# Optimization experiments

Measured on AMD Instinct MI355X. Metric: run time of the kernel, lower is better.

Reference implementation:

```python
import jax, jax.numpy as jnp
import numpy as np

P = 16
BN_EPS = 1e-5


def _to_patches(x, c, d):
    # [b, c*P, d*P] -> [b, c*d, P, P]
    b = x.shape[0]
    x = x.reshape(b, c, P, d, P).transpose(0, 1, 3, 2, 4)
    return x.reshape(b, c * d, P, P)


def _dwconv_block(x, dwk, g, bb, m, v, pwk):
    # depthwise 3x3 stride-2 conv (groups=C, no bias) + BN(eval) + GELU + 1x1 pointwise
    C = x.shape[1]
    y = jax.lax.conv_general_dilated(
        x, dwk[:, None, :, :], window_strides=(2, 2), padding=((1, 1), (1, 1)),
        feature_group_count=C, dimension_numbers=('NCHW', 'OIHW', 'NCHW'))
    y = g[None, :, None, None] * (y - m[None, :, None, None]) / jnp.sqrt(v + BN_EPS)[None, :, None, None] + bb[None, :, None, None]
    y = jax.nn.gelu(y, approximate=False)  # torch nn.GELU default = erf
    return jnp.einsum('bchw,oc->bohw', y, pwk)


def _forward(query, key, value, dw_k, bn_g, bn_b, bn_m, bn_v, pw_k, position, c1_w, c1_b, lin_w, lin_b):
    b, units, d_model = query.shape
    c = units // P
    d = d_model // P
    hp = P // 2  # spatial after stride-2 conv
    dk = hp * hp  # d_k = 64

    q = _to_patches(query, c, d)
    k = _to_patches(key, c, d)
    v = _to_patches(value, c, d)

    q = _dwconv_block(q, dw_k[0], bn_g[0], bn_b[0], bn_m[0], bn_v[0], pw_k[0])
    k = _dwconv_block(k, dw_k[1], bn_g[1], bn_b[1], bn_m[1], bn_v[1], pw_k[1])
    v = _dwconv_block(v, dw_k[2], bn_g[2], bn_b[2], bn_m[2], bn_v[2], pw_k[2])

    # [b, c*d, hp, hp] -> [b, c, d, hp*hp]
    q = q.reshape(b, c, d, dk)
    k = k.reshape(b, c, d, dk)
    v = v.reshape(b, c, d, dk)

    scores = jnp.einsum('bcdk,bcek->bcde', q, k) / jnp.sqrt(jnp.asarray(dk, q.dtype))
    scores = scores + position[None]  # learned additive position bias [c,d,d]
    p_attn = jax.nn.softmax(scores, axis=-1)
    x = jnp.einsum('bcde,bcek->bcdk', p_attn, v)  # [b, c, d, dk]

    # 'b c d (p1 p2) -> b (c p1) (d p2)', p1 = P//2
    x = x.reshape(b, c, d, hp, hp).transpose(0, 1, 3, 2, 4).reshape(b, c * hp, d * hp)

    # Conv1d(units//2 -> units, kernel 1) then Linear(d_model//2 -> d_model)
    x = jnp.einsum('bcl,oc->bol', x, c1_w) + c1_b[None, :, None]
    x = jnp.einsum('bcl,ol->bco', x, lin_w) + lin_b[None, None, :]
    return x


def setup_inputs() -> dict:
    key = jax.random.key(0)
    ks = jax.random.split(key, 8)
    b, units, d_model = 64, 32, 4096
    C = (units // P) * (d_model // P)  # 512
    inp = {
        'query': jax.random.normal(ks[0], (b, units, d_model), jnp.float32),
        'key': jax.random.normal(ks[1], (b, units, d_model), jnp.float32),
        'value': jax.random.normal(ks[2], (b, units, d_model), jnp.float32),
        'dw_k': jax.random.normal(ks[3], (3, C, 3, 3), jnp.float32) * 0.1,
        'bn_g': jnp.ones((3, C), jnp.float32),
        'bn_b': jnp.zeros((3, C), jnp.float32),
        'bn_m': jnp.zeros((3, C), jnp.float32),
        'bn_v': jnp.ones((3, C), jnp.float32),
        'pw_k': jax.random.normal(ks[4], (3, C, C), jnp.float32) * 0.02,
        'position': jax.random.normal(ks[5], (units // P, d_model // P, d_model // P), jnp.float32),
        'c1_w': jax.random.normal(ks[6], (units, units // 2), jnp.float32) * 0.1,
        'c1_b': jnp.zeros((units,), jnp.float32),
        'lin_w': jax.random.normal(ks[7], (d_model, d_model // 2), jnp.float32) * 0.02,
        'lin_b': jnp.zeros((d_model,), jnp.float32),
    }
    return inp


def reference(query, key, value, dw_k, bn_g, bn_b, bn_m, bn_v, pw_k, position, c1_w, c1_b, lin_w, lin_b):
    return _forward(query, key, value, dw_k, bn_g, bn_b, bn_m, bn_v, pw_k, position, c1_w, c1_b, lin_w, lin_b)
```

## Files before the change

kernel.cpp:

```cpp
#include <hip/hip_runtime.h>


typedef short s16x8 __attribute__((ext_vector_type(8)));
typedef float f32x4 __attribute__((ext_vector_type(4)));
typedef const __attribute__((address_space(1))) void* gas_t;
typedef __attribute__((address_space(3))) void* las_t;

__device__ __forceinline__ unsigned short f2bf(float x) {
  unsigned u = __float_as_uint(x);
  unsigned r = u + 0x7fffu + ((u >> 16) & 1u);
  return (unsigned short)(r >> 16);
}
__device__ __forceinline__ float bf2f(unsigned short h) {
  return __uint_as_float((unsigned)h << 16);
}

__global__ __launch_bounds__(256) void stageA_kernel(
    const float* __restrict__ xq, const float* __restrict__ xk,
    const float* __restrict__ xv, const float* __restrict__ dwk,
    const float* __restrict__ bng, const float* __restrict__ bnb,
    const float* __restrict__ bnm, const float* __restrict__ bnv,
    unsigned short* __restrict__ tTp)
{
  const int i  = blockIdx.y;
  const float* x = (i == 0) ? xq : (i == 1) ? xk : xv;
  const float* dwk_i = dwk + (size_t)i * 4608;
  const int co = i * 512;
  unsigned short* out = tTp + (size_t)i * 4194304;

  const int dd = threadIdx.x;
  const int oh = blockIdx.x & 7;
  const int cc = (blockIdx.x >> 3) & 1;
  const int b  = blockIdx.x >> 4;
  const int ch = cc * 256 + dd;

  float r[3][16];
#pragma unroll
  for (int kh = 0; kh < 3; ++kh) {
    int ih = 2 * oh - 1 + kh;
    if (ih >= 0 && ih <= 15) {
      const float* p = x + (size_t)(b * 32 + cc * 16 + ih) * 4096 + dd * 16;
#pragma unroll
      for (int jq = 0; jq < 4; ++jq)
        *(float4*)&r[kh][jq * 4] = *(const float4*)(p + jq * 4);
    } else {
#pragma unroll
      for (int j = 0; j < 16; ++j) r[kh][j] = 0.f;
    }
  }
  float w9[9];
#pragma unroll
  for (int j = 0; j < 9; ++j) w9[j] = dwk_i[ch * 9 + j];
  const float scale = bng[co + ch] / sqrtf(bnv[co + ch] + 1e-5f);
  const float shift = bnb[co + ch] - bnm[co + ch] * scale;

#pragma unroll
  for (int ow = 0; ow < 8; ++ow) {
    float acc = 0.f;
#pragma unroll
    for (int kh = 0; kh < 3; ++kh)
#pragma unroll
      for (int kw = 0; kw < 3; ++kw) {
        int iw = 2 * ow - 1 + kw;
        if (iw >= 0 && iw <= 15) acc = fmaf(r[kh][iw], w9[kh * 3 + kw], acc);
      }
    float y = acc * scale + shift;
    y = 0.5f * y * (1.f + erff(y * 0.70710678118654752f));
    unsigned short hi = f2bf(y);
    unsigned short lo = f2bf(y - bf2f(hi));
    size_t rowb = (size_t)(b * 64 + oh * 8 + ow) * 1024;
    out[rowb + ch] = hi;
    out[rowb + 512 + ch] = lo;
  }
}

__global__ __launch_bounds__(256) void split_kernel(
    const float* __restrict__ src, unsigned short* __restrict__ dst,
    int kshift, int total4)
{
  int i = blockIdx.x * 256 + threadIdx.x;
  if (i >= total4) return;
  size_t i4 = (size_t)i * 4;
  int K = 1 << kshift;
  int r = (int)(i4 >> kshift);
  int c = (int)(i4 & (size_t)(K - 1));
  float4 xv = *(const float4*)(src + i4);
  unsigned short h0 = f2bf(xv.x), h1 = f2bf(xv.y), h2 = f2bf(xv.z), h3 = f2bf(xv.w);
  unsigned short l0 = f2bf(xv.x - bf2f(h0)), l1 = f2bf(xv.y - bf2f(h1));
  unsigned short l2 = f2bf(xv.z - bf2f(h2)), l3 = f2bf(xv.w - bf2f(h3));
  unsigned short* dr = dst + (size_t)r * (K * 2) + c;
  uint2 hp, lp;
  hp.x = (unsigned)h0 | ((unsigned)h1 << 16);
  hp.y = (unsigned)h2 | ((unsigned)h3 << 16);
  lp.x = (unsigned)l0 | ((unsigned)l1 << 16);
  lp.y = (unsigned)l2 | ((unsigned)l3 << 16);
  *(uint2*)dr = hp;
  *(uint2*)(dr + K) = lp;
}

__global__ __launch_bounds__(256) void split_rs_kernel(
    const float* __restrict__ src, unsigned short* __restrict__ dst,
    float* __restrict__ rs, int total4)
{
  int i = blockIdx.x * 256 + threadIdx.x;
  if (i >= total4) return;
  size_t i4 = (size_t)i * 4;
  int r = (int)(i4 >> 11);
  int c = (int)(i4 & 2047);
  float4 xv = *(const float4*)(src + i4);
  unsigned short h0 = f2bf(xv.x), h1 = f2bf(xv.y), h2 = f2bf(xv.z), h3 = f2bf(xv.w);
  unsigned short l0 = f2bf(xv.x - bf2f(h0)), l1 = f2bf(xv.y - bf2f(h1));
  unsigned short l2 = f2bf(xv.z - bf2f(h2)), l3 = f2bf(xv.w - bf2f(h3));
  unsigned short* dr = dst + (size_t)r * 4096 + c;
  uint2 hp, lp;
  hp.x = (unsigned)h0 | ((unsigned)h1 << 16);
  hp.y = (unsigned)h2 | ((unsigned)h3 << 16);
  lp.x = (unsigned)l0 | ((unsigned)l1 << 16);
  lp.y = (unsigned)l2 | ((unsigned)l3 << 16);
  *(uint2*)dr = hp;
  *(uint2*)(dr + 2048) = lp;
  float s = xv.x + xv.y + xv.z + xv.w;
#pragma unroll
  for (int off = 1; off < 64; off <<= 1) s += __shfl_xor(s, off, 64);
  if ((threadIdx.x & 63) == 0) atomicAdd(&rs[r], s);
}

__global__ __launch_bounds__(256, 2) void gemm_pw_pipe_kernel(
    const unsigned short* __restrict__ Aall, const unsigned short* __restrict__ Ball,
    unsigned short* __restrict__ Call)
{
  __shared__ unsigned short lds[36864];
  const int t = threadIdx.x;

  const int flat = (blockIdx.z * 8 + blockIdx.y) * 32 + blockIdx.x;
  const int xcd = flat & 7;
  const int ii = flat >> 3;
  const int n0 = (xcd * 4 + (ii & 3)) * 128;
  const int rem = ii >> 2;
  const int m0 = (rem & 7) * 64;
  const int z = rem >> 3;

  const unsigned short* A = Aall + (size_t)z * 524288;
  const unsigned short* B = Ball + (size_t)z * 4194304;
  unsigned short* Cq = Call + (size_t)z * 4194304;

  const int K = 512, twoK = 1024, Km = 511, nt = 24;

  const int lane = t & 63;
  const int wv = t >> 6;
  const int colbase = wv * 32;
  const int h = lane & 15, g = lane >> 4;

  f32x4 acc[4][2];
#pragma unroll
  for (int mf = 0; mf < 4; ++mf)
#pragma unroll
    for (int nf = 0; nf < 2; ++nf)
      acc[mf][nf] = (f32x4){0.f, 0.f, 0.f, 0.f};

  int arow[2], ablk[2], brow[4], bblk[4];
#pragma unroll
  for (int it = 0; it < 2; ++it) {
    int s = it * 256 + t;
    arow[it] = s >> 3;
    ablk[it] = (s & 7) ^ (arow[it] & 7);
  }
#pragma unroll
  for (int it = 0; it < 4; ++it) {
    int s = it * 256 + t;
    brow[it] = s >> 3;
    bblk[it] = (s & 7) ^ (brow[it] & 7);
  }

  auto issueA = [&](int buf, int tt, int it) {
    int kp = tt * 64 + ablk[it] * 8;
    int ac = (kp < twoK) ? (kp & Km) : (kp - K);
    __builtin_amdgcn_global_load_lds(
        (gas_t)(const void*)(A + (size_t)(m0 + arow[it]) * twoK + ac),
        (las_t)(void*)((char*)lds + (buf * 24576 + it * 4096 + t * 16)), 16, 0, 0);
  };
  auto issueB = [&](int buf, int tt, int it) {
    int kp = tt * 64 + bblk[it] * 8;
    int bc = (kp < twoK) ? kp : (kp - twoK);
    __builtin_amdgcn_global_load_lds(
        (gas_t)(const void*)(B + (size_t)(n0 + brow[it]) * twoK + bc),
        (las_t)(void*)((char*)lds + (buf * 24576 + 8192 + it * 4096 + t * 16)), 16, 0, 0);
  };

  int colx[2];
  colx[0] = ((g) ^ (h & 7)) << 4;
  colx[1] = ((4 + g) ^ (h & 7)) << 4;

  auto rdA = [&](int buf, int kk, int mf) -> s16x8 {
    return *(const s16x8*)((const char*)lds +
        (buf * 24576 + (mf * 16 + h) * 128 + colx[kk]));
  };
  auto rdB = [&](int buf, int kk, int nf) -> s16x8 {
    return *(const s16x8*)((const char*)lds +
        (buf * 24576 + 8192 + (colbase + nf * 16 + h) * 128 + colx[kk]));
  };

#define MFMA8(A0, A1, A2, A3, B0, B1) \
  acc[0][0] = __builtin_amdgcn_mfma_f32_16x16x32_bf16(A0, B0, acc[0][0], 0, 0, 0); \
  acc[1][0] = __builtin_amdgcn_mfma_f32_16x16x32_bf16(A1, B0, acc[1][0], 0, 0, 0); \
  acc[2][0] = __builtin_amdgcn_mfma_f32_16x16x32_bf16(A2, B0, acc[2][0], 0, 0, 0); \
  acc[3][0] = __builtin_amdgcn_mfma_f32_16x16x32_bf16(A3, B0, acc[3][0], 0, 0, 0); \
  acc[0][1] = __builtin_amdgcn_mfma_f32_16x16x32_bf16(A0, B1, acc[0][1], 0, 0, 0); \
  acc[1][1] = __builtin_amdgcn_mfma_f32_16x16x32_bf16(A1, B1, acc[1][1], 0, 0, 0); \
  acc[2][1] = __builtin_amdgcn_mfma_f32_16x16x32_bf16(A2, B1, acc[2][1], 0, 0, 0); \
  acc[3][1] = __builtin_amdgcn_mfma_f32_16x16x32_bf16(A3, B1, acc[3][1], 0, 0, 0);

#pragma unroll
  for (int it = 0; it < 2; ++it) issueA(0, 0, it);
#pragma unroll
  for (int it = 0; it < 4; ++it) issueB(0, 0, it);
#pragma unroll
  for (int it = 0; it < 2; ++it) issueA(1, 1, it);
#pragma unroll
  for (int it = 0; it < 4; ++it) issueB(1, 1, it);
  asm volatile("s_waitcnt vmcnt(6)" ::: "memory");
  __builtin_amdgcn_sched_barrier(0);
  __builtin_amdgcn_s_barrier();
  __builtin_amdgcn_sched_barrier(0);

  int bR = 0;
  for (int tt = 0; tt <= nt - 3; ++tt) {
    const int bn2 = (bR >= 1) ? bR - 1 : 2;
    s16x8 a0 = rdA(bR, 0, 0), a1 = rdA(bR, 0, 1), a2 = rdA(bR, 0, 2), a3 = rdA(bR, 0, 3);
    s16x8 b0 = rdB(bR, 0, 0), b1 = rdB(bR, 0, 1);
    issueA(bn2, tt + 2, 0); issueA(bn2, tt + 2, 1); issueB(bn2, tt + 2, 0);
    __builtin_amdgcn_s_barrier();
    __builtin_amdgcn_s_setprio(1);
    MFMA8(a0, a1, a2, a3, b0, b1)
    __builtin_amdgcn_s_setprio(0);
    __builtin_amdgcn_s_barrier();
    a0 = rdA(bR, 1, 0); a1 = rdA(bR, 1, 1); a2 = rdA(bR, 1, 2); a3 = rdA(bR, 1, 3);
    b0 = rdB(bR, 1, 0); b1 = rdB(bR, 1, 1);
    issueB(bn2, tt + 2, 1); issueB(bn2, tt + 2, 2); issueB(bn2, tt + 2, 3);
    __builtin_amdgcn_s_barrier();
    __builtin_amdgcn_s_setprio(1);
    MFMA8(a0, a1, a2, a3, b0, b1)
    __builtin_amdgcn_s_setprio(0);
    asm volatile("s_waitcnt vmcnt(6)" ::: "memory");
    __builtin_amdgcn_sched_barrier(0);
    __builtin_amdgcn_s_barrier();
    __builtin_amdgcn_sched_barrier(0);
    bR = (bR == 2) ? 0 : bR + 1;
  }

  auto compute_tile = [&](int buf) {
#pragma unroll
    for (int kk = 0; kk < 2; ++kk) {
      s16x8 ta0 = rdA(buf, kk, 0), ta1 = rdA(buf, kk, 1);
      s16x8 ta2 = rdA(buf, kk, 2), ta3 = rdA(buf, kk, 3);
      s16x8 tb0 = rdB(buf, kk, 0), tb1 = rdB(buf, kk, 1);
      MFMA8(ta0, ta1, ta2, ta3, tb0, tb1)
    }
  };
  compute_tile(bR);
  __syncthreads();
  compute_tile((bR == 2) ? 0 : bR + 1);
#undef MFMA8

  if (z < 2) {
#pragma unroll
    for (int mf = 0; mf < 4; ++mf) {
      int mbase = m0 + mf * 16 + g * 4;
#pragma unroll
      for (int nf = 0; nf < 2; ++nf) {
        int n = n0 + colbase + nf * 16 + h;
        int bb = n >> 6, d = n & 63;
#pragma unroll
        for (int qq = 0; qq < 4; ++qq) {
          int m = mbase + qq;
          int cc = m >> 8;
          size_t rowb = ((size_t)(bb * 2 + cc) * 256 + (m & 255)) * 128;
          float vvv = acc[mf][nf][qq];
          unsigned short hi = f2bf(vvv);
          unsigned short lo = f2bf(vvv - bf2f(hi));
          Cq[rowb + d] = hi;
          Cq[rowb + 64 + d] = lo;
        }
      }
    }
  } else {
#pragma unroll
    for (int mf = 0; mf < 4; ++mf) {
      int mbase = m0 + mf * 16 + g * 4;
      int cc = mbase >> 8;
      int mc = mbase & 255;
#pragma unroll
      for (int nf = 0; nf < 2; ++nf) {
        int n = n0 + colbase + nf * 16 + h;
        int bb = n >> 6, d = n & 63;
        size_t rowb = ((size_t)(bb * 2 + cc) * 64 + d) * 512;
        ushort4 hv, lv;
        float v0 = acc[mf][nf][0], v1 = acc[mf][nf][1];
        float v2 = acc[mf][nf][2], v3 = acc[mf][nf][3];
        hv.x = f2bf(v0); hv.y = f2bf(v1); hv.z = f2bf(v2); hv.w = f2bf(v3);
        lv.x = f2bf(v0 - bf2f(hv.x)); lv.y = f2bf(v1 - bf2f(hv.y));
        lv.z = f2bf(v2 - bf2f(hv.z)); lv.w = f2bf(v3 - bf2f(hv.w));
        *(ushort4*)&Cq[rowb + mc] = hv;
        *(ushort4*)&Cq[rowb + 256 + mc] = lv;
      }
    }
  }
}

__global__ __launch_bounds__(256, 2) void gemm_final_kernel(
    const unsigned short* __restrict__ A, const unsigned short* __restrict__ B,
    float* __restrict__ C, int M, int N, int K)
{
  __shared__ unsigned short lds[36864];
  const int t = threadIdx.x;

  const int flat = blockIdx.y * 32 + blockIdx.x;
  const int xcd = flat & 7;
  const int ii = flat >> 3;
  const int n0 = (xcd * 4 + (ii & 3)) * 128;
  const int m0 = (ii >> 2) * 64;

  const int twoK = 2 * K, Km = K - 1;
  const int nt = (3 * K) >> 6;

  const int lane = t & 63;
  const int wv = t >> 6;
  const int colbase = wv * 32;
  const int h = lane & 15, g = lane >> 4;

  f32x4 acc[4][2];
#pragma unroll
  for (int mf = 0; mf < 4; ++mf)
#pragma unroll
    for (int nf = 0; nf < 2; ++nf)
      acc[mf][nf] = (f32x4){0.f, 0.f, 0.f, 0.f};

  int arow[2], ablk[2], brow[4], bblk[4];
#pragma unroll
  for (int it = 0; it < 2; ++it) {
    int s = it * 256 + t;
    arow[it] = s >> 3;
    ablk[it] = (s & 7) ^ (arow[it] & 7);
  }
#pragma unroll
  for (int it = 0; it < 4; ++it) {
    int s = it * 256 + t;
    brow[it] = s >> 3;
    bblk[it] = (s & 7) ^ (brow[it] & 7);
  }

  auto issueA = [&](int buf, int tt, int it) {
    int kp = tt * 64 + ablk[it] * 8;
    int ac = (kp < twoK) ? (kp & Km) : (kp - K);
    __builtin_amdgcn_global_load_lds(
        (gas_t)(const void*)(A + (size_t)(m0 + arow[it]) * twoK + ac),
        (las_t)(void*)((char*)lds + (buf * 24576 + it * 4096 + t * 16)), 16, 0, 0);
  };
  auto issueB = [&](int buf, int tt, int it) {
    int kp = tt * 64 + bblk[it] * 8;
    int bc = (kp < twoK) ? kp : (kp - twoK);
    __builtin_amdgcn_global_load_lds(
        (gas_t)(const void*)(B + (size_t)(n0 + brow[it]) * twoK + bc),
        (las_t)(void*)((char*)lds + (buf * 24576 + 8192 + it * 4096 + t * 16)), 16, 0, 0);
  };

  int colx[2];
  colx[0] = ((g) ^ (h & 7)) << 4;
  colx[1] = ((4 + g) ^ (h & 7)) << 4;

  auto rdA = [&](int buf, int kk, int mf) -> s16x8 {
    return *(const s16x8*)((const char*)lds +
        (buf * 24576 + (mf * 16 + h) * 128 + colx[kk]));
  };
  auto rdB = [&](int buf, int kk, int nf) -> s16x8 {
    return *(const s16x8*)((const char*)lds +
        (buf * 24576 + 8192 + (colbase + nf * 16 + h) * 128 + colx[kk]));
  };

#define MFMA8(A0, A1, A2, A3, B0, B1) \
  acc[0][0] = __builtin_amdgcn_mfma_f32_16x16x32_bf16(A0, B0, acc[0][0], 0, 0, 0); \
  acc[1][0] = __builtin_amdgcn_mfma_f32_16x16x32_bf16(A1, B0, acc[1][0], 0, 0, 0); \
  acc[2][0] = __builtin_amdgcn_mfma_f32_16x16x32_bf16(A2, B0, acc[2][0], 0, 0, 0); \
  acc[3][0] = __builtin_amdgcn_mfma_f32_16x16x32_bf16(A3, B0, acc[3][0], 0, 0, 0); \
  acc[0][1] = __builtin_amdgcn_mfma_f32_16x16x32_bf16(A0, B1, acc[0][1], 0, 0, 0); \
  acc[1][1] = __builtin_amdgcn_mfma_f32_16x16x32_bf16(A1, B1, acc[1][1], 0, 0, 0); \
  acc[2][1] = __builtin_amdgcn_mfma_f32_16x16x32_bf16(A2, B1, acc[2][1], 0, 0, 0); \
  acc[3][1] = __builtin_amdgcn_mfma_f32_16x16x32_bf16(A3, B1, acc[3][1], 0, 0, 0);

#pragma unroll
  for (int it = 0; it < 2; ++it) issueA(0, 0, it);
#pragma unroll
  for (int it = 0; it < 4; ++it) issueB(0, 0, it);
#pragma unroll
  for (int it = 0; it < 2; ++it) issueA(1, 1, it);
#pragma unroll
  for (int it = 0; it < 4; ++it) issueB(1, 1, it);
  asm volatile("s_waitcnt vmcnt(6)" ::: "memory");
  __builtin_amdgcn_sched_barrier(0);
  __builtin_amdgcn_s_barrier();
  __builtin_amdgcn_sched_barrier(0);

  int bR = 0;
  for (int tt = 0; tt <= nt - 3; ++tt) {
    const int bn2 = (bR >= 1) ? bR - 1 : 2;
    s16x8 a0 = rdA(bR, 0, 0), a1 = rdA(bR, 0, 1), a2 = rdA(bR, 0, 2), a3 = rdA(bR, 0, 3);
    s16x8 b0 = rdB(bR, 0, 0), b1 = rdB(bR, 0, 1);
    issueA(bn2, tt + 2, 0); issueA(bn2, tt + 2, 1); issueB(bn2, tt + 2, 0);
    __builtin_amdgcn_s_barrier();
    __builtin_amdgcn_s_setprio(1);
    MFMA8(a0, a1, a2, a3, b0, b1)
    __builtin_amdgcn_s_setprio(0);
    __builtin_amdgcn_s_barrier();
    a0 = rdA(bR, 1, 0); a1 = rdA(bR, 1, 1); a2 = rdA(bR, 1, 2); a3 = rdA(bR, 1, 3);
    b0 = rdB(bR, 1, 0); b1 = rdB(bR, 1, 1);
    issueB(bn2, tt + 2, 1); issueB(bn2, tt + 2, 2); issueB(bn2, tt + 2, 3);
    __builtin_amdgcn_s_barrier();
    __builtin_amdgcn_s_setprio(1);
    MFMA8(a0, a1, a2, a3, b0, b1)
    __builtin_amdgcn_s_setprio(0);
    asm volatile("s_waitcnt vmcnt(6)" ::: "memory");
    __builtin_amdgcn_sched_barrier(0);
    __builtin_amdgcn_s_barrier();
    __builtin_amdgcn_sched_barrier(0);
    bR = (bR == 2) ? 0 : bR + 1;
  }

  auto compute_tile = [&](int buf) {
#pragma unroll
    for (int kk = 0; kk < 2; ++kk) {
      s16x8 ta0 = rdA(buf, kk, 0), ta1 = rdA(buf, kk, 1);
      s16x8 ta2 = rdA(buf, kk, 2), ta3 = rdA(buf, kk, 3);
      s16x8 tb0 = rdB(buf, kk, 0), tb1 = rdB(buf, kk, 1);
      MFMA8(ta0, ta1, ta2, ta3, tb0, tb1)
    }
  };
  compute_tile(bR);
  __syncthreads();
  compute_tile((bR == 2) ? 0 : bR + 1);
#undef MFMA8

#pragma unroll
  for (int mf = 0; mf < 4; ++mf) {
    int mbase = m0 + mf * 16 + g * 4;
#pragma unroll
    for (int nf = 0; nf < 2; ++nf) {
      int n = n0 + colbase + nf * 16 + h;
#pragma unroll
      for (int qq = 0; qq < 4; ++qq)
        C[(size_t)(mbase + qq) * N + n] = acc[mf][nf][qq];
    }
  }
}

__global__ __launch_bounds__(256) void attn_mfma_kernel(
    const unsigned short* __restrict__ qp, const unsigned short* __restrict__ kp,
    const unsigned short* __restrict__ vtp, const float* __restrict__ pos,
    unsigned short* __restrict__ Xp)
{
  __shared__ char smem[59904];
  unsigned short* qs = (unsigned short*)smem;
  unsigned short* kv = (unsigned short*)(smem + 8704);
  float* sc = (float*)(smem + 26112);
  unsigned short* ps = (unsigned short*)(smem + 26112);

  const int t = threadIdx.x;
  const int rt = blockIdx.x, cc = blockIdx.y, b = blockIdx.z;
  const int i0 = rt * 32;
  const size_t qkbase = (size_t)(b * 2 + cc) * 256;
  const size_t vbase  = (size_t)(b * 2 + cc) * 64;

  const int lane = t & 63, wvv = t >> 6;
  const int h = lane & 15, g = lane >> 4;

#pragma unroll
  for (int rep = 0; rep < 2; ++rep) {
    int s = t + rep * 256;
    int row = s >> 4;
    int blk = s & 15;
    int4 val = *(const int4*)(qp + (qkbase + i0 + row) * 128 + blk * 8);
    *(int4*)((char*)qs + row * 272 + blk * 16) = val;
  }

  for (int c = 0; c < 4; ++c) {
    __syncthreads();
#pragma unroll
    for (int p2 = 0; p2 < 4; ++p2) {
      int s = t + p2 * 256;
      int row = s >> 4;
      int blk = s & 15;
      int4 val = *(const int4*)(kp + (qkbase + c * 64 + row) * 128 + blk * 8);
      *(int4*)((char*)kv + row * 272 + blk * 16) = val;
    }
    __syncthreads();
    f32x4 acc2[2];
    acc2[0] = (f32x4){0.f, 0.f, 0.f, 0.f};
    acc2[1] = (f32x4){0.f, 0.f, 0.f, 0.f};
#pragma unroll
    for (int kk = 0; kk < 6; ++kk) {
      int abase = (kk < 2) ? kk * 32 : (kk < 4) ? 64 + (kk - 2) * 32 : (kk - 4) * 32;
      int bbase = (kk < 2) ? kk * 32 : (kk < 4) ? (kk - 2) * 32 : 64 + (kk - 4) * 32;
      s16x8 bfrag = *(const s16x8*)((char*)kv + (wvv * 16 + h) * 272 + (bbase + g * 8) * 2);
#pragma unroll
      for (int mf = 0; mf < 2; ++mf) {
        s16x8 afrag = *(const s16x8*)((char*)qs + (mf * 16 + h) * 272 + (abase + g * 8) * 2);
        acc2[mf] = __builtin_amdgcn_mfma_f32_16x16x32_bf16(afrag, bfrag, acc2[mf], 0, 0, 0);
      }
    }
#pragma unroll
    for (int mf = 0; mf < 2; ++mf)
#pragma unroll
      for (int qq = 0; qq < 4; ++qq) {
        int row = mf * 16 + g * 4 + qq;
        int j = c * 64 + wvv * 16 + h;
        sc[row * 264 + j] = acc2[mf][qq] * 0.125f +
            pos[((size_t)cc * 256 + i0 + row) * 256 + j];
      }
  }
  __syncthreads();

  {
    const int r = t >> 3, j8 = t & 7;
    float e[32];
    float mx = -3.4e38f;
#pragma unroll
    for (int jj = 0; jj < 32; ++jj) {
      e[jj] = sc[r * 264 + j8 + 8 * jj];
      mx = fmaxf(mx, e[jj]);
    }
#pragma unroll
    for (int mset = 1; mset < 8; mset <<= 1) mx = fmaxf(mx, __shfl_xor(mx, mset, 64));
    float sum = 0.f;
#pragma unroll
    for (int jj = 0; jj < 32; ++jj) {
      e[jj] = expf(e[jj] - mx);
      sum += e[jj];
    }
#pragma unroll
    for (int mset = 1; mset < 8; mset <<= 1) sum += __shfl_xor(sum, mset, 64);
    float inv = 1.f / sum;
    __syncthreads();
#pragma unroll
    for (int jj = 0; jj < 32; ++jj) {
      float pv = e[jj] * inv;
      unsigned short hi = f2bf(pv);
      unsigned short lo = f2bf(pv - bf2f(hi));
      int j = j8 + 8 * jj;
      ps[r * 528 + j] = hi;
      ps[r * 528 + 264 + j] = lo;
    }
  }

  f32x4 oacc[2];
  oacc[0] = (f32x4){0.f, 0.f, 0.f, 0.f};
  oacc[1] = (f32x4){0.f, 0.f, 0.f, 0.f};
  for (int c = 0; c < 4; ++c) {
    __syncthreads();
#pragma unroll
    for (int p2 = 0; p2 < 4; ++p2) {
      int s = t + p2 * 256, row = s >> 4, blk = s & 15;
      int col = (blk < 8) ? (c * 64 + blk * 8) : (256 + c * 64 + (blk - 8) * 8);
      int4 val = *(const int4*)(vtp + (vbase + row) * 512 + col);
      *(int4*)((char*)kv + row * 272 + blk * 16) = val;
    }
    __syncthreads();
#pragma unroll
    for (int kk = 0; kk < 6; ++kk) {
      int abase = (kk < 2) ? (c * 64 + kk * 32)
                : (kk < 4) ? (264 + c * 64 + (kk - 2) * 32)
                           : (c * 64 + (kk - 4) * 32);
      int bbase = (kk < 2) ? kk * 32 : (kk < 4) ? (kk - 2) * 32 : 64 + (kk - 4) * 32;
      s16x8 bfrag = *(const s16x8*)((char*)kv + (wvv * 16 + h) * 272 + (bbase + g * 8) * 2);
#pragma unroll
      for (int mf = 0; mf < 2; ++mf) {
        s16x8 afrag = *(const s16x8*)((char*)ps + (mf * 16 + h) * 1056 + (abase + g * 8) * 2);
        oacc[mf] = __builtin_amdgcn_mfma_f32_16x16x32_bf16(afrag, bfrag, oacc[mf], 0, 0, 0);
      }
    }
  }
  {
    int Xrow = b * 16 + cc * 8 + wvv * 2 + (h >> 3);
    int c7 = h & 7;
#pragma unroll
    for (int mf = 0; mf < 2; ++mf)
#pragma unroll
      for (int qq = 0; qq < 4; ++qq) {
        int dd = i0 + mf * 16 + g * 4 + qq;
        float vvv = oacc[mf][qq];
        unsigned short hi = f2bf(vvv);
        unsigned short lo = f2bf(vvv - bf2f(hi));
        size_t base = (size_t)Xrow * 4096 + dd * 8 + c7;
        Xp[base] = hi;
        Xp[base + 2048] = lo;
      }
  }
}

__global__ __launch_bounds__(256) void epilogue_kernel(
    const float* __restrict__ G, const float* __restrict__ rs,
    const float* __restrict__ c1w, const float* __restrict__ c1b,
    const float* __restrict__ linb, float* __restrict__ out)
{
  __shared__ float W[512];
  __shared__ float Bp[32];
  const int t = threadIdx.x;
  const int ntile = blockIdx.x;
  const int b = blockIdx.y;
  W[t] = c1w[t];
  W[t + 256] = c1w[t + 256];
  if (t < 32) Bp[t] = c1b[t];
  __syncthreads();
  const int n = ntile * 256 + t;
  float gv[16];
#pragma unroll
  for (int ch = 0; ch < 16; ++ch)
    gv[ch] = G[(size_t)(b * 16 + ch) * 4096 + n];
  const float rsn = rs[n];
  const float lbn = linb[n];
#pragma unroll
  for (int o = 0; o < 32; ++o) {
    float s = lbn + Bp[o] * rsn;
#pragma unroll
    for (int ch = 0; ch < 16; ++ch) s = fmaf(W[o * 16 + ch], gv[ch], s);
    out[(size_t)(b * 32 + o) * 4096 + n] = s;
  }
}

extern "C" void kernel_launch(void* const* d_in, const int* in_sizes, int n_in,
                              void* d_out, int out_size, void* d_ws, size_t ws_size,
                              hipStream_t stream) {
  const float* q    = (const float*)d_in[0];
  const float* k    = (const float*)d_in[1];
  const float* v    = (const float*)d_in[2];
  const float* dwk  = (const float*)d_in[3];
  const float* bng  = (const float*)d_in[4];
  const float* bnb  = (const float*)d_in[5];
  const float* bnm  = (const float*)d_in[6];
  const float* bnv  = (const float*)d_in[7];
  const float* pwk  = (const float*)d_in[8];
  const float* pos  = (const float*)d_in[9];
  const float* c1w  = (const float*)d_in[10];
  const float* c1b  = (const float*)d_in[11];
  const float* linw = (const float*)d_in[12];
  const float* linb = (const float*)d_in[13];
  float* out = (float*)d_out;

  if (ws_size < 50331648u) return;

  char* ws = (char*)d_ws;
  unsigned short* qp   = (unsigned short*)(ws + 0);
  unsigned short* kpp  = (unsigned short*)(ws + 8388608);
  unsigned short* vtp  = (unsigned short*)(ws + 16777216);
  unsigned short* tTp  = (unsigned short*)(ws + 25165824);
  unsigned short* pwkp = (unsigned short*)d_out;
  unsigned short* Xp   = (unsigned short*)(ws + 25165824);
  float*          rs   = (float*)(ws + 0);
  unsigned short* lwp  = (unsigned short*)d_out;
  float*          G    = (float*)(ws + 33554432);

  split_kernel<<<768, 256, 0, stream>>>(pwk, pwkp, 9, 196608);

  stageA_kernel<<<dim3(1024, 3), 256, 0, stream>>>(
      q, k, v, dwk, bng, bnb, bnm, bnv, tTp);

  gemm_pw_pipe_kernel<<<dim3(32, 8, 3), 256, 0, stream>>>(pwkp, tTp, qp);

  attn_mfma_kernel<<<dim3(8, 2, 64), 256, 0, stream>>>(qp, kpp, vtp, pos, Xp);

  hipMemsetAsync(rs, 0, 16384, stream);
  split_rs_kernel<<<8192, 256, 0, stream>>>(linw, lwp, rs, 2097152);

  gemm_final_kernel<<<dim3(32, 16), 256, 0, stream>>>(Xp, lwp, G, 1024, 4096, 2048);

  epilogue_kernel<<<dim3(16, 64), 256, 0, stream>>>(G, rs, c1w, c1b, linb, out);
}
```

Before: 191.1 us.

## Split-K final GEMM with 64x256 tiles and double-buffered LDS pipeline

The final GEMM now uses 64x256 output tiles (each wave computes 64x64) instead of 64x128, and splits the 96 K-steps into two halves, each written to its own partial output buffer. The epilogue kernel adds the two partials. The LDS pipeline changes from three buffers to two, with prefetch issued after a barrier in the second half-step. The aim is more operand reuse per LDS read and the same grid size despite bigger tiles. In exchange it doubles the G traffic, uses more registers and a larger LDS footprint, and gives up the occupancy hint of 2 blocks per CU.

```diff
diff --git a/kernel.cpp b/kernel.cpp
--- a/kernel.cpp
+++ b/kernel.cpp
@@ -307,35 +307,37 @@
   }
 }
 
-__global__ __launch_bounds__(256, 2) void gemm_final_kernel(
+__global__ __launch_bounds__(256) void gemm_final_kernel(
     const unsigned short* __restrict__ A, const unsigned short* __restrict__ B,
-    float* __restrict__ C, int M, int N, int K)
+    float* __restrict__ C)
 {
-  __shared__ unsigned short lds[36864];
+  __shared__ unsigned short lds[40960];
   const int t = threadIdx.x;
 
   const int flat = blockIdx.y * 32 + blockIdx.x;
   const int xcd = flat & 7;
   const int ii = flat >> 3;
-  const int n0 = (xcd * 4 + (ii & 3)) * 128;
-  const int m0 = (ii >> 2) * 64;
-
-  const int twoK = 2 * K, Km = K - 1;
-  const int nt = (3 * K) >> 6;
+  const int n0 = (xcd * 2 + (ii & 1)) * 256;
+  const int rem = ii >> 1;
+  const int m0 = (rem & 15) * 64;
+  const int ks = rem >> 4;
+  const int base = ks * 48;
+
+  const int K = 2048, twoK = 4096, Km = 2047;
 
   const int lane = t & 63;
   const int wv = t >> 6;
-  const int colbase = wv * 32;
+  const int colbase = wv * 64;
   const int h = lane & 15, g = lane >> 4;
 
-  f32x4 acc[4][2];
+  f32x4 acc[4][4];
 #pragma unroll
   for (int mf = 0; mf < 4; ++mf)
 #pragma unroll
-    for (int nf = 0; nf < 2; ++nf)
+    for (int nf = 0; nf < 4; ++nf)
       acc[mf][nf] = (f32x4){0.f, 0.f, 0.f, 0.f};
 
-  int arow[2], ablk[2], brow[4], bblk[4];
+  int arow[2], ablk[2], brow[8], bblk[8];
 #pragma unroll
   for (int it = 0; it < 2; ++it) {
     int s = it * 256 + t;
@@ -343,7 +345,7 @@
     ablk[it] = (s & 7) ^ (arow[it] & 7);
   }
 #pragma unroll
-  for (int it = 0; it < 4; ++it) {
+  for (int it = 0; it < 8; ++it) {
     int s = it * 256 + t;
     brow[it] = s >> 3;
     bblk[it] = (s & 7) ^ (brow[it] & 7);
@@ -354,14 +356,14 @@
     int ac = (kp < twoK) ? (kp & Km) : (kp - K);
     __builtin_amdgcn_global_load_lds(
         (gas_t)(const void*)(A + (size_t)(m0 + arow[it]) * twoK + ac),
-        (las_t)(void*)((char*)lds + (buf * 24576 + it * 4096 + t * 16)), 16, 0, 0);
+        (las_t)(void*)((char*)lds + (buf * 40960 + it * 4096 + t * 16)), 16, 0, 0);
   };
   auto issueB = [&](int buf, int tt, int it) {
     int kp = tt * 64 + bblk[it] * 8;
     int bc = (kp < twoK) ? kp : (kp - twoK);
     __builtin_amdgcn_global_load_lds(
         (gas_t)(const void*)(B + (size_t)(n0 + brow[it]) * twoK + bc),
-        (las_t)(void*)((char*)lds + (buf * 24576 + 8192 + it * 4096 + t * 16)), 16, 0, 0);
+        (las_t)(void*)((char*)lds + (buf * 40960 + 8192 + it * 4096 + t * 16)), 16, 0, 0);
   };
 
   int colx[2];
@@ -370,84 +372,117 @@
 
   auto rdA = [&](int buf, int kk, int mf) -> s16x8 {
     return *(const s16x8*)((const char*)lds +
-        (buf * 24576 + (mf * 16 + h) * 128 + colx[kk]));
+        (buf * 40960 + (mf * 16 + h) * 128 + colx[kk]));
   };
   auto rdB = [&](int buf, int kk, int nf) -> s16x8 {
     return *(const s16x8*)((const char*)lds +
-        (buf * 24576 + 8192 + (colbase + nf * 16 + h) * 128 + colx[kk]));
-  };
-
-#define MFMA8(A0, A1, A2, A3, B0, B1) \
-  acc[0][0] = __builtin_amdgcn_mfma_f32_16x16x32_bf16(A0, B0, acc[0][0], 0, 0, 0); \
-  acc[1][0] = __builtin_amdgcn_mfma_f32_16x16x32_bf16(A1, B0, acc[1][0], 0, 0, 0); \
-  acc[2][0] = __builtin_amdgcn_mfma_f32_16x16x32_bf16(A2, B0, acc[2][0], 0, 0, 0); \
-  acc[3][0] = __builtin_amdgcn_mfma_f32_16x16x32_bf16(A3, B0, acc[3][0], 0, 0, 0); \
-  acc[0][1] = __builtin_amdgcn_mfma_f32_16x16x32_bf16(A0, B1, acc[0][1], 0, 0, 0); \
-  acc[1][1] = __builtin_amdgcn_mfma_f32_16x16x32_bf16(A1, B1, acc[1][1], 0, 0, 0); \
-  acc[2][1] = __builtin_amdgcn_mfma_f32_16x16x32_bf16(A2, B1, acc[2][1], 0, 0, 0); \
-  acc[3][1] = __builtin_amdgcn_mfma_f32_16x16x32_bf16(A3, B1, acc[3][1], 0, 0, 0);
-
-#pragma unroll
-  for (int it = 0; it < 2; ++it) issueA(0, 0, it);
-#pragma unroll
-  for (int it = 0; it < 4; ++it) issueB(0, 0, it);
-#pragma unroll
-  for (int it = 0; it < 2; ++it) issueA(1, 1, it);
-#pragma unroll
-  for (int it = 0; it < 4; ++it) issueB(1, 1, it);
-  asm volatile("s_waitcnt vmcnt(6)" ::: "memory");
+        (buf * 40960 + 8192 + (colbase + nf * 16 + h) * 128 + colx[kk]));
+  };
+
+#define MFMA16(BQ) \
+  { s16x8 a0 = rdA(BQ##buf, BQ##kk, 0), a1 = rdA(BQ##buf, BQ##kk, 1); \
+    s16x8 a2 = rdA(BQ##buf, BQ##kk, 2), a3 = rdA(BQ##buf, BQ##kk, 3); \
+    s16x8 b0 = rdB(BQ##buf, BQ##kk, 0), b1 = rdB(BQ##buf, BQ##kk, 1); \
+    s16x8 b2 = rdB(BQ##buf, BQ##kk, 2), b3 = rdB(BQ##buf, BQ##kk, 3); \
+    acc[0][0] = __builtin_amdgcn_mfma_f32_16x16x32_bf16(a0, b0, acc[0][0], 0, 0, 0); \
+    acc[1][0] = __builtin_amdgcn_mfma_f32_16x16x32_bf16(a1, b0, acc[1][0], 0, 0, 0); \
+    acc[2][0] = __builtin_amdgcn_mfma_f32_16x16x32_bf16(a2, b0, acc[2][0], 0, 0, 0); \
+    acc[3][0] = __builtin_amdgcn_mfma_f32_16x16x32_bf16(a3, b0, acc[3][0], 0, 0, 0); \
+    acc[0][1] = __builtin_amdgcn_mfma_f32_16x16x32_bf16(a0, b1, acc[0][1], 0, 0, 0); \
+    acc[1][1] = __builtin_amdgcn_mfma_f32_16x16x32_bf16(a1, b1, acc[1][1], 0, 0, 0); \
+    acc[2][1] = __builtin_amdgcn_mfma_f32_16x16x32_bf16(a2, b1, acc[2][1], 0, 0, 0); \
+    acc[3][1] = __builtin_amdgcn_mfma_f32_16x16x32_bf16(a3, b1, acc[3][1], 0, 0, 0); \
+    acc[0][2] = __builtin_amdgcn_mfma_f32_16x16x32_bf16(a0, b2, acc[0][2], 0, 0, 0); \
+    acc[1][2] = __builtin_amdgcn_mfma_f32_16x16x32_bf16(a1, b2, acc[1][2], 0, 0, 0); \
+    acc[2][2] = __builtin_amdgcn_mfma_f32_16x16x32_bf16(a2, b2, acc[2][2], 0, 0, 0); \
+    acc[3][2] = __builtin_amdgcn_mfma_f32_16x16x32_bf16(a3, b2, acc[3][2], 0, 0, 0); \
+    acc[0][3] = __builtin_amdgcn_mfma_f32_16x16x32_bf16(a0, b3, acc[0][3], 0, 0, 0); \
+    acc[1][3] = __builtin_amdgcn_mfma_f32_16x16x32_bf16(a1, b3, acc[1][3], 0, 0, 0); \
+    acc[2][3] = __builtin_amdgcn_mfma_f32_16x16x32_bf16(a2, b3, acc[2][3], 0, 0, 0); \
+    acc[3][3] = __builtin_amdgcn_mfma_f32_16x16x32_bf16(a3, b3, acc[3][3], 0, 0, 0); }
+
+#pragma unroll
+  for (int it = 0; it < 2; ++it) issueA(0, base, it);
+#pragma unroll
+  for (int it = 0; it < 8; ++it) issueB(0, base, it);
+#pragma unroll
+  for (int it = 0; it < 2; ++it) issueA(1, base + 1, it);
+#pragma unroll
+  for (int it = 0; it < 8; ++it) issueB(1, base + 1, it);
+  asm volatile("s_waitcnt vmcnt(10)" ::: "memory");
   __builtin_amdgcn_sched_barrier(0);
   __builtin_amdgcn_s_barrier();
   __builtin_amdgcn_sched_barrier(0);
 
   int bR = 0;
-  for (int tt = 0; tt <= nt - 3; ++tt) {
-    const int bn2 = (bR >= 1) ? bR - 1 : 2;
-    s16x8 a0 = rdA(bR, 0, 0), a1 = rdA(bR, 0, 1), a2 = rdA(bR, 0, 2), a3 = rdA(bR, 0, 3);
-    s16x8 b0 = rdB(bR, 0, 0), b1 = rdB(bR, 0, 1);
-    issueA(bn2, tt + 2, 0); issueA(bn2, tt + 2, 1); issueB(bn2, tt + 2, 0);
+  for (int tt = base; tt <= base + 45; ++tt) {
+    {
+      const int p0buf = bR, p0kk = 0;
+      __builtin_amdgcn_s_setprio(1);
+      MFMA16(p0)
+      __builtin_amdgcn_s_setprio(0);
+    }
     __builtin_amdgcn_s_barrier();
-    __builtin_amdgcn_s_setprio(1);
-    MFMA8(a0, a1, a2, a3, b0, b1)
-    __builtin_amdgcn_s_setprio(0);
-    __builtin_amdgcn_s_barrier();
-    a0 = rdA(bR, 1, 0); a1 = rdA(bR, 1, 1); a2 = rdA(bR, 1, 2); a3 = rdA(bR, 1, 3);
-    b0 = rdB(bR, 1, 0); b1 = rdB(bR, 1, 1);
-    issueB(bn2, tt + 2, 1); issueB(bn2, tt + 2, 2); issueB(bn2, tt + 2, 3);
-    __builtin_amdgcn_s_barrier();
-    __builtin_amdgcn_s_setprio(1);
-    MFMA8(a0, a1, a2, a3, b0, b1)
-    __builtin_amdgcn_s_setprio(0);
-    asm volatile("s_waitcnt vmcnt(6)" ::: "memory");
+    {
+      s16x8 a0 = rdA(bR, 1, 0), a1 = rdA(bR, 1, 1), a2 = rdA(bR, 1, 2), a3 = rdA(bR, 1, 3);
+      s16x8 b0 = rdB(bR, 1, 0), b1 = rdB(bR, 1, 1), b2 = rdB(bR, 1, 2), b3 = rdB(bR, 1, 3);
+      asm volatile("s_waitcnt lgkmcnt(0)" ::: "memory");
+      __builtin_amdgcn_sched_barrier(0);
+      __builtin_amdgcn_s_barrier();
+      issueA(bR, tt + 2, 0); issueA(bR, tt + 2, 1);
+#pragma unroll
+      for (int it = 0; it < 8; ++it) issueB(bR, tt + 2, it);
+      __builtin_amdgcn_s_setprio(1);
+      acc[0][0] = __builtin_amdgcn_mfma_f32_16x16x32_bf16(a0, b0, acc[0][0], 0, 0, 0);
+      acc[1][0] = __builtin_amdgcn_mfma_f32_16x16x32_bf16(a1, b0, acc[1][0], 0, 0, 0);
+      acc[2][0] = __builtin_amdgcn_mfma_f32_16x16x32_bf16(a2, b0, acc[2][0], 0, 0, 0);
+      acc[3][0] = __builtin_amdgcn_mfma_f32_16x16x32_bf16(a3, b0, acc[3][0], 0, 0, 0);
+      acc[0][1] = __builtin_amdgcn_mfma_f32_16x16x32_bf16(a0, b1, acc[0][1], 0, 0, 0);
+      acc[1][1] = __builtin_amdgcn_mfma_f32_16x16x32_bf16(a1, b1, acc[1][1], 0, 0, 0);
+      acc[2][1] = __builtin_amdgcn_mfma_f32_16x16x32_bf16(a2, b1, acc[2][1], 0, 0, 0);
+      acc[3][1] = __builtin_amdgcn_mfma_f32_16x16x32_bf16(a3, b1, acc[3][1], 0, 0, 0);
+      acc[0][2] = __builtin_amdgcn_mfma_f32_16x16x32_bf16(a0, b2, acc[0][2], 0, 0, 0);
+      acc[1][2] = __builtin_amdgcn_mfma_f32_16x16x32_bf16(a1, b2, acc[1][2], 0, 0, 0);
+      acc[2][2] = __builtin_amdgcn_mfma_f32_16x16x32_bf16(a2, b2, acc[2][2], 0, 0, 0);
+      acc[3][2] = __builtin_amdgcn_mfma_f32_16x16x32_bf16(a3, b2, acc[3][2], 0, 0, 0);
+      acc[0][3] = __builtin_amdgcn_mfma_f32_16x16x32_bf16(a0, b3, acc[0][3], 0, 0, 0);
+      acc[1][3] = __builtin_amdgcn_mfma_f32_16x16x32_bf16(a1, b3, acc[1][3], 0, 0, 0);
+      acc[2][3] = __builtin_amdgcn_mfma_f32_16x16x32_bf16(a2, b3, acc[2][3], 0, 0, 0);
+      acc[3][3] = __builtin_amdgcn_mfma_f32_16x16x32_bf16(a3, b3, acc[3][3], 0, 0, 0);
+      __builtin_amdgcn_s_setprio(0);
+    }
+    asm volatile("s_waitcnt vmcnt(10)" ::: "memory");
     __builtin_amdgcn_sched_barrier(0);
     __builtin_amdgcn_s_barrier();
     __builtin_amdgcn_sched_barrier(0);
-    bR = (bR == 2) ? 0 : bR + 1;
-  }
-
-  auto compute_tile = [&](int buf) {
-#pragma unroll
-    for (int kk = 0; kk < 2; ++kk) {
-      s16x8 ta0 = rdA(buf, kk, 0), ta1 = rdA(buf, kk, 1);
-      s16x8 ta2 = rdA(buf, kk, 2), ta3 = rdA(buf, kk, 3);
-      s16x8 tb0 = rdB(buf, kk, 0), tb1 = rdB(buf, kk, 1);
-      MFMA8(ta0, ta1, ta2, ta3, tb0, tb1)
-    }
-  };
-  compute_tile(bR);
+    bR ^= 1;
+  }
+
+  {
+    const int t0buf = bR, t0kk = 0;
+    MFMA16(t0)
+    const int t1buf = bR, t1kk = 1;
+    MFMA16(t1)
+  }
   __syncthreads();
-  compute_tile((bR == 2) ? 0 : bR + 1);
-#undef MFMA8
-
+  {
+    const int t2buf = bR ^ 1, t2kk = 0;
+    MFMA16(t2)
+    const int t3buf = bR ^ 1, t3kk = 1;
+    MFMA16(t3)
+  }
+#undef MFMA16
+
+  float* Cks = C + (size_t)ks * 4194304;
 #pragma unroll
   for (int mf = 0; mf < 4; ++mf) {
     int mbase = m0 + mf * 16 + g * 4;
 #pragma unroll
-    for (int nf = 0; nf < 2; ++nf) {
+    for (int nf = 0; nf < 4; ++nf) {
       int n = n0 + colbase + nf * 16 + h;
 #pragma unroll
       for (int qq = 0; qq < 4; ++qq)
-        C[(size_t)(mbase + qq) * N + n] = acc[mf][nf][qq];
+        Cks[(size_t)(mbase + qq) * 4096 + n] = acc[mf][nf][qq];
     }
   }
 }
@@ -612,8 +647,10 @@
   const int n = ntile * 256 + t;
   float gv[16];
 #pragma unroll
-  for (int ch = 0; ch < 16; ++ch)
-    gv[ch] = G[(size_t)(b * 16 + ch) * 4096 + n];
+  for (int ch = 0; ch < 16; ++ch) {
+    size_t off = (size_t)(b * 16 + ch) * 4096 + n;
+    gv[ch] = G[off] + G[4194304 + off];
+  }
   const float rsn = rs[n];
   const float lbn = linb[n];
 #pragma unroll
@@ -652,10 +689,10 @@
   unsigned short* vtp  = (unsigned short*)(ws + 16777216);
   unsigned short* tTp  = (unsigned short*)(ws + 25165824);
   unsigned short* pwkp = (unsigned short*)d_out;
-  unsigned short* Xp   = (unsigned short*)(ws + 25165824);
+  unsigned short* Xp   = (unsigned short*)(ws + 41943040);
   float*          rs   = (float*)(ws + 0);
   unsigned short* lwp  = (unsigned short*)d_out;
-  float*          G    = (float*)(ws + 33554432);
+  float*          G    = (float*)(ws + 8388608);
 
   split_kernel<<<768, 256, 0, stream>>>(pwk, pwkp, 9, 196608);
 
@@ -669,7 +706,7 @@
   hipMemsetAsync(rs, 0, 16384, stream);
   split_rs_kernel<<<8192, 256, 0, stream>>>(linw, lwp, rs, 2097152);
 
-  gemm_final_kernel<<<dim3(32, 16), 256, 0, stream>>>(Xp, lwp, G, 1024, 4096, 2048);
+  gemm_final_kernel<<<dim3(32, 16), 256, 0, stream>>>(Xp, lwp, G);
 
   epilogue_kernel<<<dim3(16, 64), 256, 0, stream>>>(G, rs, c1w, c1b, linb, out);
 }
```

Result: no change. 193.9 us (+1.5%).
